# Performance work log

Measured on AMD Instinct MI355X. Metric: run time of the kernel, lower is better.

Reference implementation:

```python
import jax, jax.numpy as jnp
import numpy as np

B, T, D, F, E, K = 2, 2048, 1024, 4096, 8, 2

def setup_inputs() -> dict:
    key = jax.random.key(0)
    k0, k1, k2, k3 = jax.random.split(key, 4)
    return {
        "x": jax.random.normal(k0, (B, T, D), jnp.float32),
        "Wg": jax.random.normal(k1, (D, E), jnp.float32) * (D ** -0.5),
        "W1": jax.random.normal(k2, (E, D, F), jnp.float32) * (D ** -0.5),
        "b1": jnp.zeros((E, F), jnp.float32),
        "W2": jax.random.normal(k3, (E, F, D), jnp.float32) * (F ** -0.5),
        "b2": jnp.zeros((E, D), jnp.float32),
        "topk": K,
    }

def reference(x, Wg, W1, b1, W2, b2, topk):
    n_experts = Wg.shape[-1]
    # Gating logits [B, T, E]
    gating = jnp.einsum('btd,de->bte', x, Wg)
    _, idx = jax.lax.top_k(gating, topk)
    # 0/1 mask of selected experts per token [B, T, E]
    mask = jax.nn.one_hot(idx, n_experts, dtype=x.dtype).sum(axis=-2)
    # Source does `gating -= 1/mask - 1`: no-op where mask==1, -inf where mask==0
    gate = jax.nn.softmax(jnp.where(mask > 0, gating, -jnp.inf), axis=-1)
    # Dense masked per-expert compute, exactly as the source (expert(x * mask_e))
    xm = x[:, :, None, :] * mask[:, :, :, None]          # [B, T, E, D]
    h = jax.nn.gelu(jnp.einsum('bted,edf->btef', xm, W1) + b1)  # [B, T, E, F]
    out_e = jnp.einsum('btef,efd->bted', h, W2) + b2     # [B, T, E, D]
    # Gate and sum over experts
    return jnp.sum(out_e * gate[..., None], axis=-2)      # [B, T, D]
```

## Files before the change

### kernel.cpp

```cpp
#include <hip/hip_runtime.h>
#include <hip/hip_bf16.h>
#include <math.h>

#define NB 2
#define NT 2048
#define NTOK 4096
#define DD 1024
#define FF 4096
#define NE 8
#define KSEL 2
#define BM 128
#define BN 128
#define BK 64
#define ROWCAP 9216
#define ROWTILES 72
#define KP2 2

typedef __attribute__((ext_vector_type(8))) short short8_t;
typedef __attribute__((ext_vector_type(4))) float f32x4;

__device__ __forceinline__ unsigned short f2bf(float f){
  unsigned u = __float_as_uint(f);
  unsigned r = (u + 0x7fffu + ((u >> 16) & 1u)) >> 16;
  return (unsigned short)r;
}

__device__ __forceinline__ int xcd_swz(int lin, int nwg){
  int q = nwg >> 3, r = nwg & 7;
  int xcd = lin & 7, idx = lin >> 3;
  return (xcd < r ? xcd * (q + 1) : r * (q + 1) + (xcd - r) * q) + idx;
}

#define GLOAD_LDS(g, l) \
  __builtin_amdgcn_global_load_lds((const __attribute__((address_space(1))) void*)(g), \
                                   (__attribute__((address_space(3))) void*)(l), 16, 0, 0)


__global__ void k_prep(const float* __restrict__ x, const float* __restrict__ wg,
                       short* __restrict__ xb, int* __restrict__ topk_idx,
                       float* __restrict__ topk_gate, int* __restrict__ counts){
  int wid = threadIdx.x >> 6, lane = threadIdx.x & 63;
  int t = blockIdx.x * 4 + wid;
  const float* xr = x + (size_t)t * DD;
  short* xbr = xb + (size_t)t * DD;
  double acc[NE];
#pragma unroll
  for (int e = 0; e < NE; ++e) acc[e] = 0.0;
#pragma unroll
  for (int p = 0; p < 4; ++p){
    int d = p * 256 + lane * 4;
    float4 v = *(const float4*)(xr + d);
    short4 o;
    o.x = (short)f2bf(v.x); o.y = (short)f2bf(v.y);
    o.z = (short)f2bf(v.z); o.w = (short)f2bf(v.w);
    *(short4*)(xbr + d) = o;
    const float* w0 = wg + (size_t)d * NE;
    float vv[4] = {v.x, v.y, v.z, v.w};
#pragma unroll
    for (int j = 0; j < 4; ++j){
      double xv = (double)vv[j];
#pragma unroll
      for (int e = 0; e < NE; ++e) acc[e] += xv * (double)w0[j * NE + e];
    }
  }
#pragma unroll
  for (int e = 0; e < NE; ++e){
#pragma unroll
    for (int s = 32; s; s >>= 1) acc[e] += __shfl_xor(acc[e], s, 64);
  }
  if (lane == 0){
    int i0 = 0; double v0 = acc[0];
#pragma unroll
    for (int e = 1; e < NE; ++e) if (acc[e] > v0){ v0 = acc[e]; i0 = e; }
    int i1 = -1; double v1 = -1e300;
#pragma unroll
    for (int e = 0; e < NE; ++e) if (e != i0 && acc[e] > v1){ v1 = acc[e]; i1 = e; }
    double g0 = 1.0 / (1.0 + exp(v1 - v0));
    topk_idx[2 * t] = i0; topk_idx[2 * t + 1] = i1;
    topk_gate[2 * t] = (float)g0; topk_gate[2 * t + 1] = (float)(1.0 - g0);
    atomicAdd(&counts[i0], 1);
    atomicAdd(&counts[i1], 1);
  }
}


__global__ void k_transpose_all(const float* __restrict__ W1, const float* __restrict__ W2,
                                short* __restrict__ w1t, short* __restrict__ w2t){
  __shared__ short T[64][132];
  int id = blockIdx.x;
  bool isW2 = id >= 4096;
  int rem = id & 4095;
  int e = rem >> 9;
  int tr = rem & 511;
  int R, C, c0, r0;
  const float* in; short* out;
  if (!isW2){ R = DD; C = FF; c0 = (tr & 63) * 64; r0 = (tr >> 6) * 128;
              in = W1 + (size_t)e * R * C; out = w1t + (size_t)e * R * C; }
  else      { R = FF; C = DD; c0 = (tr & 15) * 64; r0 = (tr >> 4) * 128;
              in = W2 + (size_t)e * R * C; out = w2t + (size_t)e * R * C; }
  int t = threadIdx.x;
  int rr = t >> 4, c4 = (t & 15) * 4;
#pragma unroll
  for (int p = 0; p < 8; ++p){
    int row = p * 16 + rr;
    float4 v = *(const float4*)(in + (size_t)(r0 + row) * C + c0 + c4);
    T[c4 + 0][row] = (short)f2bf(v.x);
    T[c4 + 1][row] = (short)f2bf(v.y);
    T[c4 + 2][row] = (short)f2bf(v.z);
    T[c4 + 3][row] = (short)f2bf(v.w);
  }
  __syncthreads();
  int c8 = (t & 15) * 8;
#pragma unroll
  for (int q = 0; q < 4; ++q){
    int orow = q * 16 + rr;
    short4 lo = *(const short4*)&T[orow][c8];
    short4 hi = *(const short4*)&T[orow][c8 + 4];
    short8_t w;
    w[0] = lo.x; w[1] = lo.y; w[2] = lo.z; w[3] = lo.w;
    w[4] = hi.x; w[5] = hi.y; w[6] = hi.z; w[7] = hi.w;
    *(short8_t*)(out + (size_t)(c0 + orow) * R + r0 + c8) = w;
  }
}


__global__ void k_route_all(const int* __restrict__ counts, const int* __restrict__ topk_idx,
                            const float* __restrict__ topk_gate, int* __restrict__ poff_g,
                            int* __restrict__ row_token, float* __restrict__ row_gate,
                            int* __restrict__ slot_of){
  __shared__ int poff[NE + 1], cur[NE], rends[NE];
  if (threadIdx.x == 0){
    int off = 0;
    for (int e = 0; e < NE; ++e){
      poff[e] = off; cur[e] = off; rends[e] = off + counts[e];
      off += (counts[e] + BM - 1) & ~(BM - 1);
    }
    poff[NE] = off;
    for (int e = 0; e <= NE; ++e) poff_g[e] = poff[e];
  }
  __syncthreads();
  for (int t = threadIdx.x; t < NTOK; t += 256){
#pragma unroll
    for (int k = 0; k < KSEL; ++k){
      int e = topk_idx[2 * t + k];
      float g = topk_gate[2 * t + k];
      int slot = atomicAdd(&cur[e], 1);
      row_token[slot] = t;
      row_gate[slot] = g;
      slot_of[2 * t + k] = slot;
    }
  }
  __syncthreads();
#pragma unroll
  for (int e = 0; e < NE; ++e)
    for (int s = rends[e] + (int)threadIdx.x; s < poff[e + 1]; s += 256){
      row_token[s] = 0; row_gate[s] = 0.f;
    }
}


__launch_bounds__(256, 4)
__global__ void k_gemm1(const short* __restrict__ xb, const short* __restrict__ w1t,
                        const float* __restrict__ b1, short* __restrict__ h,
                        const int* __restrict__ row_token, const int* __restrict__ poff){
  __shared__ short As[BM * BK];
  __shared__ short Bs[BN * BK];
  int wg = xcd_swz(blockIdx.x, ROWTILES * (FF / BN));
  int g = wg >> 6, t6 = wg & 63;
  int bx = (g >> 2) * 8 + (t6 & 7);
  int by = (g & 3) * 8 + (t6 >> 3);
  int row0 = bx * BM;
  if (row0 >= poff[NE]) return;
  int e = 0;
  while (row0 >= poff[e + 1]) ++e;
  int n0 = by * BN;
  int tid = threadIdx.x;

  const short* asrc[4]; const short* bsrc[4];
#pragma unroll
  for (int p = 0; p < 4; ++p){
    int L = p * 256 + tid;
    int r = L >> 3, cs = L & 7;
    int cd = cs ^ (r & 7);
    int tok = row_token[row0 + r];
    asrc[p] = xb + (size_t)tok * DD + cd * 8;
    bsrc[p] = w1t + (size_t)e * FF * DD + (size_t)(n0 + r) * DD + cd * 8;
  }
  short* alds = As + tid * 8;
  short* blds = Bs + tid * 8;

  f32x4 acc[4][4];
#pragma unroll
  for (int i = 0; i < 4; ++i)
#pragma unroll
    for (int j = 0; j < 4; ++j) acc[i][j] = (f32x4){0.f, 0.f, 0.f, 0.f};

  int wid = tid >> 6, lane = tid & 63;
  int wr = wid >> 1, wc = wid & 1;
  int lrow = lane & 15, lk = lane >> 4;

  for (int k0 = 0; k0 < DD; k0 += BK){
#pragma unroll
    for (int p = 0; p < 4; ++p){
      GLOAD_LDS(asrc[p] + k0, alds + p * 2048);
      GLOAD_LDS(bsrc[p] + k0, blds + p * 2048);
    }
    __syncthreads();
#pragma unroll
    for (int kk = 0; kk < 2; ++kk){
      short8_t a[4], b[4];
      int c = kk * 4 + lk;
#pragma unroll
      for (int m = 0; m < 4; ++m){
        int r = wr * 64 + m * 16 + lrow;
        a[m] = *(const short8_t*)(As + r * BK + ((c ^ (r & 7)) * 8));
      }
#pragma unroll
      for (int n = 0; n < 4; ++n){
        int r = wc * 64 + n * 16 + lrow;
        b[n] = *(const short8_t*)(Bs + r * BK + ((c ^ (r & 7)) * 8));
      }
#pragma unroll
      for (int m = 0; m < 4; ++m)
#pragma unroll
        for (int n = 0; n < 4; ++n)
          acc[m][n] = __builtin_amdgcn_mfma_f32_16x16x32_bf16(a[m], b[n], acc[m][n], 0, 0, 0);
    }
    __syncthreads();
  }

  const float* b1e = b1 + (size_t)e * FF;
  float bias[4];
#pragma unroll
  for (int n = 0; n < 4; ++n) bias[n] = b1e[n0 + wc * 64 + n * 16 + lrow];
#pragma unroll
  for (int m = 0; m < 4; ++m){
#pragma unroll
    for (int j = 0; j < 4; ++j){
      int row = row0 + wr * 64 + m * 16 + lk * 4 + j;
      short* hr = h + (size_t)row * FF + n0 + wc * 64 + lrow;
#pragma unroll
      for (int n = 0; n < 4; ++n){
        float v = acc[m][n][j] + bias[n];
        float u = 0.7978845608028654f * (v + 0.044715f * v * v * v);
        float gl = v / (1.0f + __expf(-2.0f * u));
        hr[n * 16] = (short)f2bf(gl);
      }
    }
  }
}


__launch_bounds__(256, 4)
__global__ void k_gemm2(const short* __restrict__ h, const short* __restrict__ w2t,
                        const float* __restrict__ b2, float* __restrict__ ya,
                        float* __restrict__ yb, const int* __restrict__ poff){
  __shared__ short As[BM * BK];
  __shared__ short Bs[BN * BK];
  int wg = xcd_swz(blockIdx.x, ROWTILES * (DD / BN) * KP2);
  int kz = wg / (ROWTILES * (DD / BN));
  int c5 = wg % (ROWTILES * (DD / BN));
  int g = c5 >> 5, t5 = c5 & 31;
  int bx = g * 4 + (t5 & 3);
  int by = t5 >> 2;
  int row0 = bx * BM;
  if (row0 >= poff[NE]) return;
  int e = 0;
  while (row0 >= poff[e + 1]) ++e;
  int n0 = by * BN;
  int tid = threadIdx.x;

  const short* asrc[4]; const short* bsrc[4];
#pragma unroll
  for (int p = 0; p < 4; ++p){
    int L = p * 256 + tid;
    int r = L >> 3, cs = L & 7;
    int cd = cs ^ (r & 7);
    asrc[p] = h + (size_t)(row0 + r) * FF + cd * 8;
    bsrc[p] = w2t + (size_t)e * DD * FF + (size_t)(n0 + r) * FF + cd * 8;
  }
  short* alds = As + tid * 8;
  short* blds = Bs + tid * 8;

  f32x4 acc[4][4];
#pragma unroll
  for (int i = 0; i < 4; ++i)
#pragma unroll
    for (int j = 0; j < 4; ++j) acc[i][j] = (f32x4){0.f, 0.f, 0.f, 0.f};

  int wid = tid >> 6, lane = tid & 63;
  int wr = wid >> 1, wc = wid & 1;
  int lrow = lane & 15, lk = lane >> 4;

  int kbeg = kz * (FF / KP2), kend = kbeg + FF / KP2;
  for (int k0 = kbeg; k0 < kend; k0 += BK){
#pragma unroll
    for (int p = 0; p < 4; ++p){
      GLOAD_LDS(asrc[p] + k0, alds + p * 2048);
      GLOAD_LDS(bsrc[p] + k0, blds + p * 2048);
    }
    __syncthreads();
#pragma unroll
    for (int kk = 0; kk < 2; ++kk){
      short8_t a[4], b[4];
      int c = kk * 4 + lk;
#pragma unroll
      for (int m = 0; m < 4; ++m){
        int r = wr * 64 + m * 16 + lrow;
        a[m] = *(const short8_t*)(As + r * BK + ((c ^ (r & 7)) * 8));
      }
#pragma unroll
      for (int n = 0; n < 4; ++n){
        int r = wc * 64 + n * 16 + lrow;
        b[n] = *(const short8_t*)(Bs + r * BK + ((c ^ (r & 7)) * 8));
      }
#pragma unroll
      for (int m = 0; m < 4; ++m)
#pragma unroll
        for (int n = 0; n < 4; ++n)
          acc[m][n] = __builtin_amdgcn_mfma_f32_16x16x32_bf16(a[m], b[n], acc[m][n], 0, 0, 0);
    }
    __syncthreads();
  }

  float* y = (kz == 0) ? ya : yb;
  const float* b2e = b2 + (size_t)e * DD;
  float bias[4];
#pragma unroll
  for (int n = 0; n < 4; ++n) bias[n] = (kz == 0) ? b2e[n0 + wc * 64 + n * 16 + lrow] : 0.0f;
#pragma unroll
  for (int m = 0; m < 4; ++m){
#pragma unroll
    for (int j = 0; j < 4; ++j){
      int row = row0 + wr * 64 + m * 16 + lk * 4 + j;
      float* yr = y + (size_t)row * DD + n0 + wc * 64 + lrow;
#pragma unroll
      for (int n = 0; n < 4; ++n)
        yr[n * 16] = acc[m][n][j] + bias[n];
    }
  }
}


__global__ void k_combine(const float* __restrict__ ya, const float* __restrict__ yb,
                          const int* __restrict__ slot_of, const float* __restrict__ topk_gate,
                          float* __restrict__ out){
  int i = blockIdx.x * 256 + threadIdx.x;
  int t = i >> 8;
  int c4 = (i & 255) * 4;
  int s0 = slot_of[2 * t], s1 = slot_of[2 * t + 1];
  float g0 = topk_gate[2 * t], g1 = topk_gate[2 * t + 1];
  float4 a0 = *(const float4*)(ya + (size_t)s0 * DD + c4);
  float4 b0 = *(const float4*)(yb + (size_t)s0 * DD + c4);
  float4 a1 = *(const float4*)(ya + (size_t)s1 * DD + c4);
  float4 b1 = *(const float4*)(yb + (size_t)s1 * DD + c4);
  float4 o;
  o.x = g0 * (a0.x + b0.x) + g1 * (a1.x + b1.x);
  o.y = g0 * (a0.y + b0.y) + g1 * (a1.y + b1.y);
  o.z = g0 * (a0.z + b0.z) + g1 * (a1.z + b1.z);
  o.w = g0 * (a0.w + b0.w) + g1 * (a1.w + b1.w);
  *(float4*)(out + (size_t)t * DD + c4) = o;
}


extern "C" void kernel_launch(void* const* d_in, const int* in_sizes, int n_in,
                              void* d_out, int out_size, void* d_ws, size_t ws_size,
                              hipStream_t stream){
  (void)in_sizes; (void)n_in; (void)out_size; (void)ws_size;
  const float* x  = (const float*)d_in[0];
  const float* Wg = (const float*)d_in[1];
  const float* W1 = (const float*)d_in[2];
  const float* b1 = (const float*)d_in[3];
  const float* W2 = (const float*)d_in[4];
  const float* b2 = (const float*)d_in[5];
  float* out = (float*)d_out;
  char* ws = (char*)d_ws;

  int*   counts    = (int*)(ws + 0);
  int*   poff      = (int*)(ws + 256);
  int*   topk_idx  = (int*)(ws + 1024);
  float* topk_gate = (float*)(ws + 33792);
  int*   row_token = (int*)(ws + 66560);
  float* row_gate  = (float*)(ws + 103424);
  int*   slot_of   = (int*)(ws + 140288);
  short* xb        = (short*)(ws + 173056);
  short* w1t       = (short*)(ws + 8561664);
  short* w2t       = (short*)(ws + 75670528);
  short* h         = (short*)(ws + 142779392);
  float* ya        = (float*)(ws + 173056);
  float* yb        = (float*)(ws + 37921792);

  hipMemsetAsync(counts, 0, 32, stream);

  k_prep<<<dim3(NTOK / 4), 256, 0, stream>>>(x, Wg, xb, topk_idx, topk_gate, counts);
  k_transpose_all<<<dim3(8192), 256, 0, stream>>>(W1, W2, w1t, w2t);
  k_route_all<<<dim3(1), 256, 0, stream>>>(counts, topk_idx, topk_gate, poff,
                                           row_token, row_gate, slot_of);
  k_gemm1<<<dim3(ROWTILES * (FF / BN)), 256, 0, stream>>>(xb, w1t, b1, h, row_token, poff);
  k_gemm2<<<dim3(ROWTILES * (DD / BN) * KP2), 256, 0, stream>>>(h, w2t, b2, ya, yb, poff);
  k_combine<<<dim3(NTOK * DD / 4 / 256), 256, 0, stream>>>(ya, yb, slot_of, topk_gate, out);
}
```

Baseline: 470.1 us.

## Double-buffer 128x256 MFMA GEMMs and fuse gated combine via atomics

Both expert GEMMs move to 512-thread blocks with 128x256 tiles and double-buffered LDS. Global-to-LDS loads for the next K-slice are split across the sub-steps and issued while MFMAs run on the current buffer, with raw barriers, sched barriers and setprio controlling the order. The second GEMM now applies the gate and scatters straight into the output with float atomicAdd, which removes the ya/yb buffers and the separate combine kernel. The cost is a memset of the output, atomic contention from two split-K halves and two experts per token, non-deterministic summation order, and more LDS per block.

```diff
diff --git a/kernel.cpp b/kernel.cpp
--- a/kernel.cpp
+++ b/kernel.cpp
@@ -10,7 +10,7 @@
 #define NE 8
 #define KSEL 2
 #define BM 128
-#define BN 128
+#define BN 256
 #define BK 64
 #define ROWCAP 9216
 #define ROWTILES 72
@@ -34,6 +34,34 @@
 #define GLOAD_LDS(g, l) \
   __builtin_amdgcn_global_load_lds((const __attribute__((address_space(1))) void*)(g), \
                                    (__attribute__((address_space(3))) void*)(l), 16, 0, 0)
+
+#define VMCNT0 asm volatile("s_waitcnt vmcnt(0)" ::: "memory")
+#define LGKM0  asm volatile("s_waitcnt lgkmcnt(0)" ::: "memory")
+#define SCHEDB __builtin_amdgcn_sched_barrier(0)
+#define RAWBAR __builtin_amdgcn_s_barrier()
+
+__device__ __forceinline__ void mfma16(f32x4 acc[4][4], const short8_t* a, const short8_t* b){
+#pragma unroll
+  for (int m = 0; m < 4; ++m)
+#pragma unroll
+    for (int n = 0; n < 4; ++n)
+      acc[m][n] = __builtin_amdgcn_mfma_f32_16x16x32_bf16(a[m], b[n], acc[m][n], 0, 0, 0);
+}
+
+__device__ __forceinline__ void read_frags(const short* A, const short* B, int wr, int wc,
+                                           int lrow, int lk, int kk, short8_t* a, short8_t* b){
+  int c = kk * 4 + lk;
+#pragma unroll
+  for (int m = 0; m < 4; ++m){
+    int r = wr * 64 + m * 16 + lrow;
+    a[m] = *(const short8_t*)(A + r * 64 + ((c ^ (r & 7)) * 8));
+  }
+#pragma unroll
+  for (int n = 0; n < 4; ++n){
+    int r = wc * 64 + n * 16 + lrow;
+    b[n] = *(const short8_t*)(B + r * 64 + ((c ^ (r & 7)) * 8));
+  }
+}
 
 
 __global__ void k_prep(const float* __restrict__ x, const float* __restrict__ wg,
@@ -126,8 +154,8 @@
 
 __global__ void k_route_all(const int* __restrict__ counts, const int* __restrict__ topk_idx,
                             const float* __restrict__ topk_gate, int* __restrict__ poff_g,
-                            int* __restrict__ row_token, float* __restrict__ row_gate,
-                            int* __restrict__ slot_of){
+                            int* __restrict__ rend_g, int* __restrict__ row_token,
+                            float* __restrict__ row_gate){
   __shared__ int poff[NE + 1], cur[NE], rends[NE];
   if (threadIdx.x == 0){
     int off = 0;
@@ -137,6 +165,7 @@
     }
     poff[NE] = off;
     for (int e = 0; e <= NE; ++e) poff_g[e] = poff[e];
+    for (int e = 0; e < NE; ++e) rend_g[e] = rends[e];
   }
   __syncthreads();
   for (int t = threadIdx.x; t < NTOK; t += 256){
@@ -147,7 +176,6 @@
       int slot = atomicAdd(&cur[e], 1);
       row_token[slot] = t;
       row_gate[slot] = g;
-      slot_of[2 * t + k] = slot;
     }
   }
   __syncthreads();
@@ -159,16 +187,16 @@
 }
 
 
-__launch_bounds__(256, 4)
+__launch_bounds__(512, 2)
 __global__ void k_gemm1(const short* __restrict__ xb, const short* __restrict__ w1t,
                         const float* __restrict__ b1, short* __restrict__ h,
                         const int* __restrict__ row_token, const int* __restrict__ poff){
-  __shared__ short As[BM * BK];
-  __shared__ short Bs[BN * BK];
+  __shared__ short As[2][BM * BK];
+  __shared__ short Bs[2][BN * BK];
   int wg = xcd_swz(blockIdx.x, ROWTILES * (FF / BN));
-  int g = wg >> 6, t6 = wg & 63;
-  int bx = (g >> 2) * 8 + (t6 & 7);
-  int by = (g & 3) * 8 + (t6 >> 3);
+  int g = wg >> 5, t5 = wg & 31;
+  int bx = (g >> 2) * 8 + (t5 & 7);
+  int by = (g & 3) * 4 + (t5 >> 3);
   int row0 = bx * BM;
   if (row0 >= poff[NE]) return;
   int e = 0;
@@ -176,18 +204,20 @@
   int n0 = by * BN;
   int tid = threadIdx.x;
 
-  const short* asrc[4]; const short* bsrc[4];
+  const short* a_src[2]; const short* b_src[4];
+#pragma unroll
+  for (int p = 0; p < 2; ++p){
+    int L = p * 512 + tid;
+    int r = L >> 3, cd = (L & 7) ^ (r & 7);
+    int tok = row_token[row0 + r];
+    a_src[p] = xb + (size_t)tok * DD + cd * 8;
+  }
 #pragma unroll
   for (int p = 0; p < 4; ++p){
-    int L = p * 256 + tid;
-    int r = L >> 3, cs = L & 7;
-    int cd = cs ^ (r & 7);
-    int tok = row_token[row0 + r];
-    asrc[p] = xb + (size_t)tok * DD + cd * 8;
-    bsrc[p] = w1t + (size_t)e * FF * DD + (size_t)(n0 + r) * DD + cd * 8;
-  }
-  short* alds = As + tid * 8;
-  short* blds = Bs + tid * 8;
+    int L = p * 512 + tid;
+    int r = L >> 3, cd = (L & 7) ^ (r & 7);
+    b_src[p] = w1t + (size_t)e * FF * DD + (size_t)(n0 + r) * DD + cd * 8;
+  }
 
   f32x4 acc[4][4];
 #pragma unroll
@@ -196,37 +226,58 @@
     for (int j = 0; j < 4; ++j) acc[i][j] = (f32x4){0.f, 0.f, 0.f, 0.f};
 
   int wid = tid >> 6, lane = tid & 63;
-  int wr = wid >> 1, wc = wid & 1;
+  int wr = wid >> 2, wc = wid & 3;
   int lrow = lane & 15, lk = lane >> 4;
 
-  for (int k0 = 0; k0 < DD; k0 += BK){
-#pragma unroll
-    for (int p = 0; p < 4; ++p){
-      GLOAD_LDS(asrc[p] + k0, alds + p * 2048);
-      GLOAD_LDS(bsrc[p] + k0, blds + p * 2048);
-    }
-    __syncthreads();
-#pragma unroll
-    for (int kk = 0; kk < 2; ++kk){
-      short8_t a[4], b[4];
-      int c = kk * 4 + lk;
-#pragma unroll
-      for (int m = 0; m < 4; ++m){
-        int r = wr * 64 + m * 16 + lrow;
-        a[m] = *(const short8_t*)(As + r * BK + ((c ^ (r & 7)) * 8));
-      }
-#pragma unroll
-      for (int n = 0; n < 4; ++n){
-        int r = wc * 64 + n * 16 + lrow;
-        b[n] = *(const short8_t*)(Bs + r * BK + ((c ^ (r & 7)) * 8));
-      }
-#pragma unroll
-      for (int m = 0; m < 4; ++m)
-#pragma unroll
-        for (int n = 0; n < 4; ++n)
-          acc[m][n] = __builtin_amdgcn_mfma_f32_16x16x32_bf16(a[m], b[n], acc[m][n], 0, 0, 0);
-    }
-    __syncthreads();
+#define STAGE1_FIRST(B, K0)  { GLOAD_LDS(a_src[0] + (K0), &As[B][0] + tid * 8); \
+                               GLOAD_LDS(a_src[1] + (K0), &As[B][0] + 4096 + tid * 8); \
+                               GLOAD_LDS(b_src[0] + (K0), &Bs[B][0] + tid * 8); }
+#define STAGE1_SECOND(B, K0) { GLOAD_LDS(b_src[1] + (K0), &Bs[B][0] + 4096 + tid * 8); \
+                               GLOAD_LDS(b_src[2] + (K0), &Bs[B][0] + 8192 + tid * 8); \
+                               GLOAD_LDS(b_src[3] + (K0), &Bs[B][0] + 12288 + tid * 8); }
+
+  STAGE1_FIRST(0, 0); STAGE1_SECOND(0, 0);
+  VMCNT0; RAWBAR; SCHEDB;
+
+  const int NITER = (DD / BK) / 2;
+#pragma unroll 1
+  for (int it = 0; it < NITER; ++it){
+    int k0 = it * 2 * BK;
+    bool more = (it < NITER - 1);
+    {
+      STAGE1_FIRST(1, k0 + BK);
+      short8_t a[4], b[4];
+      read_frags(&As[0][0], &Bs[0][0], wr, wc, lrow, lk, 0, a, b);
+      LGKM0; SCHEDB;
+      __builtin_amdgcn_s_setprio(1); mfma16(acc, a, b); __builtin_amdgcn_s_setprio(0);
+      RAWBAR; SCHEDB;
+    }
+    {
+      STAGE1_SECOND(1, k0 + BK);
+      short8_t a[4], b[4];
+      read_frags(&As[0][0], &Bs[0][0], wr, wc, lrow, lk, 1, a, b);
+      LGKM0; SCHEDB;
+      __builtin_amdgcn_s_setprio(1); mfma16(acc, a, b); __builtin_amdgcn_s_setprio(0);
+      VMCNT0;
+      RAWBAR; SCHEDB;
+    }
+    {
+      if (more) STAGE1_FIRST(0, k0 + 2 * BK);
+      short8_t a[4], b[4];
+      read_frags(&As[1][0], &Bs[1][0], wr, wc, lrow, lk, 0, a, b);
+      LGKM0; SCHEDB;
+      __builtin_amdgcn_s_setprio(1); mfma16(acc, a, b); __builtin_amdgcn_s_setprio(0);
+      RAWBAR; SCHEDB;
+    }
+    {
+      if (more) STAGE1_SECOND(0, k0 + 2 * BK);
+      short8_t a[4], b[4];
+      read_frags(&As[1][0], &Bs[1][0], wr, wc, lrow, lk, 1, a, b);
+      LGKM0; SCHEDB;
+      __builtin_amdgcn_s_setprio(1); mfma16(acc, a, b); __builtin_amdgcn_s_setprio(0);
+      if (more) VMCNT0;
+      RAWBAR; SCHEDB;
+    }
   }
 
   const float* b1e = b1 + (size_t)e * FF;
@@ -251,36 +302,39 @@
 }
 
 
-__launch_bounds__(256, 4)
+__launch_bounds__(512, 2)
 __global__ void k_gemm2(const short* __restrict__ h, const short* __restrict__ w2t,
-                        const float* __restrict__ b2, float* __restrict__ ya,
-                        float* __restrict__ yb, const int* __restrict__ poff){
-  __shared__ short As[BM * BK];
-  __shared__ short Bs[BN * BK];
+                        const float* __restrict__ b2, float* __restrict__ out,
+                        const int* __restrict__ row_token, const float* __restrict__ row_gate,
+                        const int* __restrict__ poff, const int* __restrict__ rend){
+  __shared__ short As[2][BM * BK];
+  __shared__ short Bs[2][BN * BK];
   int wg = xcd_swz(blockIdx.x, ROWTILES * (DD / BN) * KP2);
-  int kz = wg / (ROWTILES * (DD / BN));
-  int c5 = wg % (ROWTILES * (DD / BN));
-  int g = c5 >> 5, t5 = c5 & 31;
-  int bx = g * 4 + (t5 & 3);
-  int by = t5 >> 2;
+  int g = wg >> 5, t5 = wg & 31;
+  int bx = (g % 9) * 8 + (t5 & 7);
+  int kz = g / 9;
+  int by = t5 >> 3;
   int row0 = bx * BM;
   if (row0 >= poff[NE]) return;
   int e = 0;
   while (row0 >= poff[e + 1]) ++e;
   int n0 = by * BN;
   int tid = threadIdx.x;
-
-  const short* asrc[4]; const short* bsrc[4];
+  int kbeg = kz * (FF / KP2);
+
+  const short* a_src[2]; const short* b_src[4];
+#pragma unroll
+  for (int p = 0; p < 2; ++p){
+    int L = p * 512 + tid;
+    int r = L >> 3, cd = (L & 7) ^ (r & 7);
+    a_src[p] = h + (size_t)(row0 + r) * FF + kbeg + cd * 8;
+  }
 #pragma unroll
   for (int p = 0; p < 4; ++p){
-    int L = p * 256 + tid;
-    int r = L >> 3, cs = L & 7;
-    int cd = cs ^ (r & 7);
-    asrc[p] = h + (size_t)(row0 + r) * FF + cd * 8;
-    bsrc[p] = w2t + (size_t)e * DD * FF + (size_t)(n0 + r) * FF + cd * 8;
-  }
-  short* alds = As + tid * 8;
-  short* blds = Bs + tid * 8;
+    int L = p * 512 + tid;
+    int r = L >> 3, cd = (L & 7) ^ (r & 7);
+    b_src[p] = w2t + (size_t)e * DD * FF + (size_t)(n0 + r) * FF + kbeg + cd * 8;
+  }
 
   f32x4 acc[4][4];
 #pragma unroll
@@ -289,77 +343,74 @@
     for (int j = 0; j < 4; ++j) acc[i][j] = (f32x4){0.f, 0.f, 0.f, 0.f};
 
   int wid = tid >> 6, lane = tid & 63;
-  int wr = wid >> 1, wc = wid & 1;
+  int wr = wid >> 2, wc = wid & 3;
   int lrow = lane & 15, lk = lane >> 4;
 
-  int kbeg = kz * (FF / KP2), kend = kbeg + FF / KP2;
-  for (int k0 = kbeg; k0 < kend; k0 += BK){
-#pragma unroll
-    for (int p = 0; p < 4; ++p){
-      GLOAD_LDS(asrc[p] + k0, alds + p * 2048);
-      GLOAD_LDS(bsrc[p] + k0, blds + p * 2048);
-    }
-    __syncthreads();
-#pragma unroll
-    for (int kk = 0; kk < 2; ++kk){
-      short8_t a[4], b[4];
-      int c = kk * 4 + lk;
-#pragma unroll
-      for (int m = 0; m < 4; ++m){
-        int r = wr * 64 + m * 16 + lrow;
-        a[m] = *(const short8_t*)(As + r * BK + ((c ^ (r & 7)) * 8));
-      }
-#pragma unroll
-      for (int n = 0; n < 4; ++n){
-        int r = wc * 64 + n * 16 + lrow;
-        b[n] = *(const short8_t*)(Bs + r * BK + ((c ^ (r & 7)) * 8));
-      }
-#pragma unroll
-      for (int m = 0; m < 4; ++m)
-#pragma unroll
-        for (int n = 0; n < 4; ++n)
-          acc[m][n] = __builtin_amdgcn_mfma_f32_16x16x32_bf16(a[m], b[n], acc[m][n], 0, 0, 0);
-    }
-    __syncthreads();
-  }
-
-  float* y = (kz == 0) ? ya : yb;
+  STAGE1_FIRST(0, 0); STAGE1_SECOND(0, 0);
+  VMCNT0; RAWBAR; SCHEDB;
+
+  const int NITER2 = (FF / KP2 / BK) / 2;
+#pragma unroll 1
+  for (int it = 0; it < NITER2; ++it){
+    int k0 = it * 2 * BK;
+    bool more = (it < NITER2 - 1);
+    {
+      STAGE1_FIRST(1, k0 + BK);
+      short8_t a[4], b[4];
+      read_frags(&As[0][0], &Bs[0][0], wr, wc, lrow, lk, 0, a, b);
+      LGKM0; SCHEDB;
+      __builtin_amdgcn_s_setprio(1); mfma16(acc, a, b); __builtin_amdgcn_s_setprio(0);
+      RAWBAR; SCHEDB;
+    }
+    {
+      STAGE1_SECOND(1, k0 + BK);
+      short8_t a[4], b[4];
+      read_frags(&As[0][0], &Bs[0][0], wr, wc, lrow, lk, 1, a, b);
+      LGKM0; SCHEDB;
+      __builtin_amdgcn_s_setprio(1); mfma16(acc, a, b); __builtin_amdgcn_s_setprio(0);
+      VMCNT0;
+      RAWBAR; SCHEDB;
+    }
+    {
+      if (more) STAGE1_FIRST(0, k0 + 2 * BK);
+      short8_t a[4], b[4];
+      read_frags(&As[1][0], &Bs[1][0], wr, wc, lrow, lk, 0, a, b);
+      LGKM0; SCHEDB;
+      __builtin_amdgcn_s_setprio(1); mfma16(acc, a, b); __builtin_amdgcn_s_setprio(0);
+      RAWBAR; SCHEDB;
+    }
+    {
+      if (more) STAGE1_SECOND(0, k0 + 2 * BK);
+      short8_t a[4], b[4];
+      read_frags(&As[1][0], &Bs[1][0], wr, wc, lrow, lk, 1, a, b);
+      LGKM0; SCHEDB;
+      __builtin_amdgcn_s_setprio(1); mfma16(acc, a, b); __builtin_amdgcn_s_setprio(0);
+      if (more) VMCNT0;
+      RAWBAR; SCHEDB;
+    }
+  }
+
+  int rende = rend[e];
   const float* b2e = b2 + (size_t)e * DD;
   float bias[4];
 #pragma unroll
-  for (int n = 0; n < 4; ++n) bias[n] = (kz == 0) ? b2e[n0 + wc * 64 + n * 16 + lrow] : 0.0f;
+  for (int n = 0; n < 4; ++n)
+    bias[n] = (kz == 0) ? b2e[n0 + wc * 64 + n * 16 + lrow] : 0.0f;
 #pragma unroll
   for (int m = 0; m < 4; ++m){
 #pragma unroll
     for (int j = 0; j < 4; ++j){
       int row = row0 + wr * 64 + m * 16 + lk * 4 + j;
-      float* yr = y + (size_t)row * DD + n0 + wc * 64 + lrow;
-#pragma unroll
-      for (int n = 0; n < 4; ++n)
-        yr[n * 16] = acc[m][n][j] + bias[n];
-    }
-  }
-}
-
-
-__global__ void k_combine(const float* __restrict__ ya, const float* __restrict__ yb,
-                          const int* __restrict__ slot_of, const float* __restrict__ topk_gate,
-                          float* __restrict__ out){
-  int i = blockIdx.x * 256 + threadIdx.x;
-  int t = i >> 8;
-  int c4 = (i & 255) * 4;
-  int s0 = slot_of[2 * t], s1 = slot_of[2 * t + 1];
-  float g0 = topk_gate[2 * t], g1 = topk_gate[2 * t + 1];
-  float4 a0 = *(const float4*)(ya + (size_t)s0 * DD + c4);
-  float4 b0 = *(const float4*)(yb + (size_t)s0 * DD + c4);
-  float4 a1 = *(const float4*)(ya + (size_t)s1 * DD + c4);
-  float4 b1 = *(const float4*)(yb + (size_t)s1 * DD + c4);
-  float4 o;
-  o.x = g0 * (a0.x + b0.x) + g1 * (a1.x + b1.x);
-  o.y = g0 * (a0.y + b0.y) + g1 * (a1.y + b1.y);
-  o.z = g0 * (a0.z + b0.z) + g1 * (a1.z + b1.z);
-  o.w = g0 * (a0.w + b0.w) + g1 * (a1.w + b1.w);
-  *(float4*)(out + (size_t)t * DD + c4) = o;
+      if (row < rende){
+        int tok = row_token[row];
+        float gt = row_gate[row];
+        float* orow = out + (size_t)tok * DD + n0 + wc * 64 + lrow;
+#pragma unroll
+        for (int n = 0; n < 4; ++n)
+          atomicAdd(&orow[n * 16], gt * (acc[m][n][j] + bias[n]));
+      }
+    }
+  }
 }
 
 
@@ -378,25 +429,24 @@
 
   int*   counts    = (int*)(ws + 0);
   int*   poff      = (int*)(ws + 256);
+  int*   rend      = (int*)(ws + 512);
   int*   topk_idx  = (int*)(ws + 1024);
   float* topk_gate = (float*)(ws + 33792);
   int*   row_token = (int*)(ws + 66560);
   float* row_gate  = (float*)(ws + 103424);
-  int*   slot_of   = (int*)(ws + 140288);
-  short* xb        = (short*)(ws + 173056);
-  short* w1t       = (short*)(ws + 8561664);
-  short* w2t       = (short*)(ws + 75670528);
-  short* h         = (short*)(ws + 142779392);
-  float* ya        = (float*)(ws + 173056);
-  float* yb        = (float*)(ws + 37921792);
+  short* xb        = (short*)(ws + 140288);
+  short* w1t       = (short*)(ws + 8528896);
+  short* w2t       = (short*)(ws + 75637760);
+  short* h         = (short*)(ws + 142746624);
 
   hipMemsetAsync(counts, 0, 32, stream);
+  hipMemsetAsync(out, 0, (size_t)NTOK * DD * sizeof(float), stream);
 
   k_prep<<<dim3(NTOK / 4), 256, 0, stream>>>(x, Wg, xb, topk_idx, topk_gate, counts);
   k_transpose_all<<<dim3(8192), 256, 0, stream>>>(W1, W2, w1t, w2t);
-  k_route_all<<<dim3(1), 256, 0, stream>>>(counts, topk_idx, topk_gate, poff,
-                                           row_token, row_gate, slot_of);
-  k_gemm1<<<dim3(ROWTILES * (FF / BN)), 256, 0, stream>>>(xb, w1t, b1, h, row_token, poff);
-  k_gemm2<<<dim3(ROWTILES * (DD / BN) * KP2), 256, 0, stream>>>(h, w2t, b2, ya, yb, poff);
-  k_combine<<<dim3(NTOK * DD / 4 / 256), 256, 0, stream>>>(ya, yb, slot_of, topk_gate, out);
-}
+  k_route_all<<<dim3(1), 256, 0, stream>>>(counts, topk_idx, topk_gate, poff, rend,
+                                           row_token, row_gate);
+  k_gemm1<<<dim3(ROWTILES * (FF / BN)), 512, 0, stream>>>(xb, w1t, b1, h, row_token, poff);
+  k_gemm2<<<dim3(ROWTILES * (DD / BN) * KP2), 512, 0, stream>>>(h, w2t, b2, out,
+                                                                row_token, row_gate, poff, rend);
+}
```

Result: slower. 550.5 us (+17.1%).

## Use 256x256 double-buffered GEMM tiles with fused bf16 conversion of x

Applied to the files above, without the earlier changes.

Both expert GEMMs move from 128x128 single-buffered tiles to 256x256 tiles with 512 threads. They double-buffer LDS, interleave the next tile's loads with MFMA phases, and raise wave priority around the MFMA blocks. GEMM1 now reads fp32 x directly and converts it to bf16 while writing to LDS, which removes the separate bf16 x buffer written in prep. GEMM2's split-K now runs as two sequential launches where the second adds into one output buffer, so combine reads a single y array. Expert padding grows to 256 rows, which adds wasted rows, and the larger tiles cut occupancy and the number of workgroups.

```diff
diff --git a/kernel.cpp b/kernel.cpp
--- a/kernel.cpp
+++ b/kernel.cpp
@@ -2,27 +2,22 @@
 #include <hip/hip_bf16.h>
 #include <math.h>
 
-#define NB 2
-#define NT 2048
 #define NTOK 4096
 #define DD 1024
 #define FF 4096
 #define NE 8
 #define KSEL 2
-#define BM 128
-#define BN 128
 #define BK 64
-#define ROWCAP 9216
-#define ROWTILES 72
-#define KP2 2
+#define PADR 256
+#define ROWCAP 10240
+#define MT 40
 
 typedef __attribute__((ext_vector_type(8))) short short8_t;
 typedef __attribute__((ext_vector_type(4))) float f32x4;
 
 __device__ __forceinline__ unsigned short f2bf(float f){
   unsigned u = __float_as_uint(f);
-  unsigned r = (u + 0x7fffu + ((u >> 16) & 1u)) >> 16;
-  return (unsigned short)r;
+  return (unsigned short)((u + 0x7fffu + ((u >> 16) & 1u)) >> 16);
 }
 
 __device__ __forceinline__ int xcd_swz(int lin, int nwg){
@@ -34,15 +29,19 @@
 #define GLOAD_LDS(g, l) \
   __builtin_amdgcn_global_load_lds((const __attribute__((address_space(1))) void*)(g), \
                                    (__attribute__((address_space(3))) void*)(l), 16, 0, 0)
+#define WAIT_VL asm volatile("s_waitcnt vmcnt(0) lgkmcnt(0)" ::: "memory")
+#define WAIT_V  asm volatile("s_waitcnt vmcnt(0)" ::: "memory")
+#define RAWBAR __builtin_amdgcn_s_barrier()
+#define PRIO1 __builtin_amdgcn_s_setprio(1)
+#define PRIO0 __builtin_amdgcn_s_setprio(0)
 
 
 __global__ void k_prep(const float* __restrict__ x, const float* __restrict__ wg,
-                       short* __restrict__ xb, int* __restrict__ topk_idx,
-                       float* __restrict__ topk_gate, int* __restrict__ counts){
+                       int* __restrict__ topk_idx, float* __restrict__ topk_gate,
+                       int* __restrict__ counts){
   int wid = threadIdx.x >> 6, lane = threadIdx.x & 63;
   int t = blockIdx.x * 4 + wid;
   const float* xr = x + (size_t)t * DD;
-  short* xbr = xb + (size_t)t * DD;
   double acc[NE];
 #pragma unroll
   for (int e = 0; e < NE; ++e) acc[e] = 0.0;
@@ -50,10 +49,6 @@
   for (int p = 0; p < 4; ++p){
     int d = p * 256 + lane * 4;
     float4 v = *(const float4*)(xr + d);
-    short4 o;
-    o.x = (short)f2bf(v.x); o.y = (short)f2bf(v.y);
-    o.z = (short)f2bf(v.z); o.w = (short)f2bf(v.w);
-    *(short4*)(xbr + d) = o;
     const float* w0 = wg + (size_t)d * NE;
     float vv[4] = {v.x, v.y, v.z, v.w};
 #pragma unroll
@@ -126,14 +121,13 @@
 
 __global__ void k_route_all(const int* __restrict__ counts, const int* __restrict__ topk_idx,
                             const float* __restrict__ topk_gate, int* __restrict__ poff_g,
-                            int* __restrict__ row_token, float* __restrict__ row_gate,
-                            int* __restrict__ slot_of){
+                            int* __restrict__ row_token, int* __restrict__ slot_of){
   __shared__ int poff[NE + 1], cur[NE], rends[NE];
   if (threadIdx.x == 0){
     int off = 0;
     for (int e = 0; e < NE; ++e){
       poff[e] = off; cur[e] = off; rends[e] = off + counts[e];
-      off += (counts[e] + BM - 1) & ~(BM - 1);
+      off += (counts[e] + PADR - 1) & ~(PADR - 1);
     }
     poff[NE] = off;
     for (int e = 0; e <= NE; ++e) poff_g[e] = poff[e];
@@ -143,90 +137,131 @@
 #pragma unroll
     for (int k = 0; k < KSEL; ++k){
       int e = topk_idx[2 * t + k];
-      float g = topk_gate[2 * t + k];
       int slot = atomicAdd(&cur[e], 1);
       row_token[slot] = t;
-      row_gate[slot] = g;
       slot_of[2 * t + k] = slot;
     }
   }
   __syncthreads();
 #pragma unroll
   for (int e = 0; e < NE; ++e)
-    for (int s = rends[e] + (int)threadIdx.x; s < poff[e + 1]; s += 256){
-      row_token[s] = 0; row_gate[s] = 0.f;
-    }
-}
-
-
-__launch_bounds__(256, 4)
-__global__ void k_gemm1(const short* __restrict__ xb, const short* __restrict__ w1t,
+    for (int s = rends[e] + (int)threadIdx.x; s < poff[e + 1]; s += 256)
+      row_token[s] = 0;
+}
+
+
+__launch_bounds__(512, 2)
+__global__ void k_gemm1(const float* __restrict__ x, const short* __restrict__ w1t,
                         const float* __restrict__ b1, short* __restrict__ h,
                         const int* __restrict__ row_token, const int* __restrict__ poff){
-  __shared__ short As[BM * BK];
-  __shared__ short Bs[BN * BK];
-  int wg = xcd_swz(blockIdx.x, ROWTILES * (FF / BN));
-  int g = wg >> 6, t6 = wg & 63;
-  int bx = (g >> 2) * 8 + (t6 & 7);
-  int by = (g & 3) * 8 + (t6 >> 3);
-  int row0 = bx * BM;
+  __shared__ short As[2][2][8192];
+  __shared__ short Bs[2][2][8192];
+  int lin = xcd_swz(blockIdx.x, MT * (FF / 256));
+  int by = lin / MT, bx = lin % MT;
+  int row0 = bx * 256;
   if (row0 >= poff[NE]) return;
   int e = 0;
   while (row0 >= poff[e + 1]) ++e;
-  int n0 = by * BN;
+  int n0 = by * 256;
   int tid = threadIdx.x;
-
-  const short* asrc[4]; const short* bsrc[4];
+  int wid = tid >> 6, lane = tid & 63;
+  int wr = wid >> 2, wc = wid & 3;
+  int lrow = lane & 15, lk = lane >> 4;
+
+  const short* bsrc[2];
+#pragma unroll
+  for (int p = 0; p < 2; ++p){
+    int L = p * 512 + tid;
+    int r = L >> 3, cd = (L & 7) ^ (r & 7);
+    bsrc[p] = w1t + (size_t)e * FF * DD + (size_t)(n0 + r) * DD + cd * 8;
+  }
+  const float* asrc[2][4];
+  int aelem[4];
 #pragma unroll
   for (int p = 0; p < 4; ++p){
-    int L = p * 256 + tid;
-    int r = L >> 3, cs = L & 7;
-    int cd = cs ^ (r & 7);
-    int tok = row_token[row0 + r];
-    asrc[p] = xb + (size_t)tok * DD + cd * 8;
-    bsrc[p] = w1t + (size_t)e * FF * DD + (size_t)(n0 + r) * DD + cd * 8;
-  }
-  short* alds = As + tid * 8;
-  short* blds = Bs + tid * 8;
-
-  f32x4 acc[4][4];
-#pragma unroll
-  for (int i = 0; i < 4; ++i)
+    int q = p * 512 + tid;
+    int r = q >> 4, c4 = (q & 15) * 4;
+    aelem[p] = r * 64 + (((c4 >> 3) ^ (r & 7)) << 3) + (c4 & 7);
+#pragma unroll
+    for (int h2 = 0; h2 < 2; ++h2){
+      int tok = row_token[row0 + h2 * 128 + r];
+      asrc[h2][p] = x + (size_t)tok * DD + c4;
+    }
+  }
+
+  f32x4 acc[8][4];
+#pragma unroll
+  for (int i = 0; i < 8; ++i)
 #pragma unroll
     for (int j = 0; j < 4; ++j) acc[i][j] = (f32x4){0.f, 0.f, 0.f, 0.f};
 
-  int wid = tid >> 6, lane = tid & 63;
-  int wr = wid >> 1, wc = wid & 1;
-  int lrow = lane & 15, lk = lane >> 4;
-
-  for (int k0 = 0; k0 < DD; k0 += BK){
+  auto rdA = [&](const short* A0, int mq, int kk, short8_t* av){
+#pragma unroll
+    for (int m = 0; m < 4; ++m){
+      int r = mq * 64 + m * 16 + lrow;
+      av[m] = *(const short8_t*)(A0 + r * 64 + (((kk * 4 + lk) ^ (r & 7)) << 3));
+    }
+  };
+  auto rdB = [&](const short* B0, int kk, short8_t* bv){
+#pragma unroll
+    for (int n = 0; n < 4; ++n){
+      int r = (wc & 1) * 64 + n * 16 + lrow;
+      bv[n] = *(const short8_t*)(B0 + r * 64 + (((kk * 4 + lk) ^ (r & 7)) << 3));
+    }
+  };
+  auto MF = [&](int mq, short8_t* av, short8_t* bv){
+#pragma unroll
+    for (int m = 0; m < 4; ++m)
+#pragma unroll
+      for (int n = 0; n < 4; ++n)
+        acc[mq * 4 + m][n] = __builtin_amdgcn_mfma_f32_16x16x32_bf16(av[m], bv[n], acc[mq * 4 + m][n], 0, 0, 0);
+  };
+  auto aload = [&](float4* f, int h2, int k0){
+#pragma unroll
+    for (int p = 0; p < 4; ++p) f[p] = *(const float4*)(asrc[h2][p] + k0);
+  };
+  auto awrite = [&](float4* f, int nb, int h2){
+    short* dst = &As[nb][h2][0];
 #pragma unroll
     for (int p = 0; p < 4; ++p){
-      GLOAD_LDS(asrc[p] + k0, alds + p * 2048);
-      GLOAD_LDS(bsrc[p] + k0, blds + p * 2048);
-    }
-    __syncthreads();
-#pragma unroll
-    for (int kk = 0; kk < 2; ++kk){
-      short8_t a[4], b[4];
-      int c = kk * 4 + lk;
-#pragma unroll
-      for (int m = 0; m < 4; ++m){
-        int r = wr * 64 + m * 16 + lrow;
-        a[m] = *(const short8_t*)(As + r * BK + ((c ^ (r & 7)) * 8));
-      }
-#pragma unroll
-      for (int n = 0; n < 4; ++n){
-        int r = wc * 64 + n * 16 + lrow;
-        b[n] = *(const short8_t*)(Bs + r * BK + ((c ^ (r & 7)) * 8));
-      }
-#pragma unroll
-      for (int m = 0; m < 4; ++m)
-#pragma unroll
-        for (int n = 0; n < 4; ++n)
-          acc[m][n] = __builtin_amdgcn_mfma_f32_16x16x32_bf16(a[m], b[n], acc[m][n], 0, 0, 0);
-    }
-    __syncthreads();
+      short4 cv;
+      cv.x = (short)f2bf(f[p].x); cv.y = (short)f2bf(f[p].y);
+      cv.z = (short)f2bf(f[p].z); cv.w = (short)f2bf(f[p].w);
+      *(short4*)(dst + aelem[p]) = cv;
+    }
+  };
+  auto bstage = [&](int nb, int h2, int k0){
+    GLOAD_LDS(bsrc[0] + (size_t)h2 * 128 * DD + k0, &Bs[nb][h2][0] + tid * 8);
+    GLOAD_LDS(bsrc[1] + (size_t)h2 * 128 * DD + k0, &Bs[nb][h2][0] + 4096 + tid * 8);
+  };
+
+  float4 fa[4], fc[4];
+  aload(fa, 0, 0); aload(fc, 1, 0);
+  bstage(0, 0, 0); bstage(0, 1, 0);
+  awrite(fa, 0, 0); awrite(fc, 0, 1);
+  WAIT_VL; RAWBAR;
+
+#pragma unroll 1
+  for (int kt = 0; kt < DD / BK; ++kt){
+    int buf = kt & 1, nb = buf ^ 1;
+    int k1 = (kt + 1) * BK;
+    bool more = (kt + 1 < DD / BK);
+    const short* A0 = &As[buf][wr][0];
+    const short* B0 = &Bs[buf][wc >> 1][0];
+    short8_t av[4], bv[4];
+    if (more){ aload(fa, 0, k1); bstage(nb, 0, k1); }
+    rdB(B0, 0, bv); rdA(A0, 0, 0, av);
+    RAWBAR; PRIO1; MF(0, av, bv); PRIO0; RAWBAR;
+    if (more){ aload(fc, 1, k1); bstage(nb, 1, k1); }
+    rdA(A0, 1, 0, av);
+    RAWBAR; PRIO1; MF(1, av, bv); PRIO0; RAWBAR;
+    if (more) awrite(fa, nb, 0);
+    rdB(B0, 1, bv); rdA(A0, 0, 1, av);
+    RAWBAR; PRIO1; MF(0, av, bv); PRIO0; RAWBAR;
+    if (more) awrite(fc, nb, 1);
+    rdA(A0, 1, 1, av);
+    RAWBAR; PRIO1; MF(1, av, bv); PRIO0;
+    WAIT_VL; RAWBAR;
   }
 
   const float* b1e = b1 + (size_t)e * FF;
@@ -234,14 +269,14 @@
 #pragma unroll
   for (int n = 0; n < 4; ++n) bias[n] = b1e[n0 + wc * 64 + n * 16 + lrow];
 #pragma unroll
-  for (int m = 0; m < 4; ++m){
+  for (int mi = 0; mi < 8; ++mi){
 #pragma unroll
     for (int j = 0; j < 4; ++j){
-      int row = row0 + wr * 64 + m * 16 + lk * 4 + j;
+      int row = row0 + wr * 128 + mi * 16 + lk * 4 + j;
       short* hr = h + (size_t)row * FF + n0 + wc * 64 + lrow;
 #pragma unroll
       for (int n = 0; n < 4; ++n){
-        float v = acc[m][n][j] + bias[n];
+        float v = acc[mi][n][j] + bias[n];
         float u = 0.7978845608028654f * (v + 0.044715f * v * v * v);
         float gl = v / (1.0f + __expf(-2.0f * u));
         hr[n * 16] = (short)f2bf(gl);
@@ -251,114 +286,131 @@
 }
 
 
-__launch_bounds__(256, 4)
-__global__ void k_gemm2(const short* __restrict__ h, const short* __restrict__ w2t,
-                        const float* __restrict__ b2, float* __restrict__ ya,
-                        float* __restrict__ yb, const int* __restrict__ poff){
-  __shared__ short As[BM * BK];
-  __shared__ short Bs[BN * BK];
-  int wg = xcd_swz(blockIdx.x, ROWTILES * (DD / BN) * KP2);
-  int kz = wg / (ROWTILES * (DD / BN));
-  int c5 = wg % (ROWTILES * (DD / BN));
-  int g = c5 >> 5, t5 = c5 & 31;
-  int bx = g * 4 + (t5 & 3);
-  int by = t5 >> 2;
-  int row0 = bx * BM;
+__launch_bounds__(512, 2)
+__global__ void k_gemm2(const short* __restrict__ hA, const short* __restrict__ w2t,
+                        const float* __restrict__ b2, float* __restrict__ y,
+                        const int* __restrict__ poff, int kbeg, int am){
+  __shared__ short As[2][2][8192];
+  __shared__ short Bs[2][2][8192];
+  int lin = xcd_swz(blockIdx.x, MT * (DD / 256));
+  int by = lin / MT, bx = lin % MT;
+  int row0 = bx * 256;
   if (row0 >= poff[NE]) return;
   int e = 0;
   while (row0 >= poff[e + 1]) ++e;
-  int n0 = by * BN;
+  int n0 = by * 256;
   int tid = threadIdx.x;
-
-  const short* asrc[4]; const short* bsrc[4];
-#pragma unroll
-  for (int p = 0; p < 4; ++p){
-    int L = p * 256 + tid;
-    int r = L >> 3, cs = L & 7;
-    int cd = cs ^ (r & 7);
-    asrc[p] = h + (size_t)(row0 + r) * FF + cd * 8;
-    bsrc[p] = w2t + (size_t)e * DD * FF + (size_t)(n0 + r) * FF + cd * 8;
-  }
-  short* alds = As + tid * 8;
-  short* blds = Bs + tid * 8;
-
-  f32x4 acc[4][4];
-#pragma unroll
-  for (int i = 0; i < 4; ++i)
+  int wid = tid >> 6, lane = tid & 63;
+  int wr = wid >> 2, wc = wid & 3;
+  int lrow = lane & 15, lk = lane >> 4;
+
+  const short* asrc[2]; const short* bsrc[2];
+#pragma unroll
+  for (int p = 0; p < 2; ++p){
+    int L = p * 512 + tid;
+    int r = L >> 3, cd = (L & 7) ^ (r & 7);
+    asrc[p] = hA + (size_t)(row0 + r) * FF + kbeg + cd * 8;
+    bsrc[p] = w2t + (size_t)e * DD * FF + (size_t)(n0 + r) * FF + kbeg + cd * 8;
+  }
+
+  f32x4 acc[8][4];
+#pragma unroll
+  for (int i = 0; i < 8; ++i)
 #pragma unroll
     for (int j = 0; j < 4; ++j) acc[i][j] = (f32x4){0.f, 0.f, 0.f, 0.f};
 
-  int wid = tid >> 6, lane = tid & 63;
-  int wr = wid >> 1, wc = wid & 1;
-  int lrow = lane & 15, lk = lane >> 4;
-
-  int kbeg = kz * (FF / KP2), kend = kbeg + FF / KP2;
-  for (int k0 = kbeg; k0 < kend; k0 += BK){
-#pragma unroll
-    for (int p = 0; p < 4; ++p){
-      GLOAD_LDS(asrc[p] + k0, alds + p * 2048);
-      GLOAD_LDS(bsrc[p] + k0, blds + p * 2048);
-    }
-    __syncthreads();
-#pragma unroll
-    for (int kk = 0; kk < 2; ++kk){
-      short8_t a[4], b[4];
-      int c = kk * 4 + lk;
-#pragma unroll
-      for (int m = 0; m < 4; ++m){
-        int r = wr * 64 + m * 16 + lrow;
-        a[m] = *(const short8_t*)(As + r * BK + ((c ^ (r & 7)) * 8));
+  auto rdA = [&](const short* A0, int mq, int kk, short8_t* av){
+#pragma unroll
+    for (int m = 0; m < 4; ++m){
+      int r = mq * 64 + m * 16 + lrow;
+      av[m] = *(const short8_t*)(A0 + r * 64 + (((kk * 4 + lk) ^ (r & 7)) << 3));
+    }
+  };
+  auto rdB = [&](const short* B0, int kk, short8_t* bv){
+#pragma unroll
+    for (int n = 0; n < 4; ++n){
+      int r = (wc & 1) * 64 + n * 16 + lrow;
+      bv[n] = *(const short8_t*)(B0 + r * 64 + (((kk * 4 + lk) ^ (r & 7)) << 3));
+    }
+  };
+  auto MF = [&](int mq, short8_t* av, short8_t* bv){
+#pragma unroll
+    for (int m = 0; m < 4; ++m)
+#pragma unroll
+      for (int n = 0; n < 4; ++n)
+        acc[mq * 4 + m][n] = __builtin_amdgcn_mfma_f32_16x16x32_bf16(av[m], bv[n], acc[mq * 4 + m][n], 0, 0, 0);
+  };
+  auto astage = [&](int nb, int h2, int k0){
+    GLOAD_LDS(asrc[0] + (size_t)h2 * 128 * FF + k0, &As[nb][h2][0] + tid * 8);
+    GLOAD_LDS(asrc[1] + (size_t)h2 * 128 * FF + k0, &As[nb][h2][0] + 4096 + tid * 8);
+  };
+  auto bstage = [&](int nb, int h2, int k0){
+    GLOAD_LDS(bsrc[0] + (size_t)h2 * 128 * FF + k0, &Bs[nb][h2][0] + tid * 8);
+    GLOAD_LDS(bsrc[1] + (size_t)h2 * 128 * FF + k0, &Bs[nb][h2][0] + 4096 + tid * 8);
+  };
+
+  astage(0, 0, 0); astage(0, 1, 0);
+  bstage(0, 0, 0); bstage(0, 1, 0);
+  WAIT_V; RAWBAR;
+
+  const int NKT = 2048 / BK;
+#pragma unroll 1
+  for (int kt = 0; kt < NKT; ++kt){
+    int buf = kt & 1, nb = buf ^ 1;
+    int k1 = (kt + 1) * BK;
+    bool more = (kt + 1 < NKT);
+    const short* A0 = &As[buf][wr][0];
+    const short* B0 = &Bs[buf][wc >> 1][0];
+    short8_t av[4], bv[4];
+    if (more){ astage(nb, 0, k1); bstage(nb, 0, k1); }
+    rdB(B0, 0, bv); rdA(A0, 0, 0, av);
+    RAWBAR; PRIO1; MF(0, av, bv); PRIO0; RAWBAR;
+    if (more){ astage(nb, 1, k1); bstage(nb, 1, k1); }
+    rdA(A0, 1, 0, av);
+    RAWBAR; PRIO1; MF(1, av, bv); PRIO0; RAWBAR;
+    rdB(B0, 1, bv); rdA(A0, 0, 1, av);
+    RAWBAR; PRIO1; MF(0, av, bv); PRIO0; RAWBAR;
+    rdA(A0, 1, 1, av);
+    RAWBAR; PRIO1; MF(1, av, bv); PRIO0;
+    WAIT_V; RAWBAR;
+  }
+
+  float bias[4];
+  const float* b2e = b2 + (size_t)e * DD;
+#pragma unroll
+  for (int n = 0; n < 4; ++n) bias[n] = b2e[n0 + wc * 64 + n * 16 + lrow];
+#pragma unroll
+  for (int mi = 0; mi < 8; ++mi){
+#pragma unroll
+    for (int j = 0; j < 4; ++j){
+      int row = row0 + wr * 128 + mi * 16 + lk * 4 + j;
+      float* yr = y + (size_t)row * DD + n0 + wc * 64 + lrow;
+      if (am){
+#pragma unroll
+        for (int n = 0; n < 4; ++n) yr[n * 16] += acc[mi][n][j];
+      } else {
+#pragma unroll
+        for (int n = 0; n < 4; ++n) yr[n * 16] = acc[mi][n][j] + bias[n];
       }
-#pragma unroll
-      for (int n = 0; n < 4; ++n){
-        int r = wc * 64 + n * 16 + lrow;
-        b[n] = *(const short8_t*)(Bs + r * BK + ((c ^ (r & 7)) * 8));
-      }
-#pragma unroll
-      for (int m = 0; m < 4; ++m)
-#pragma unroll
-        for (int n = 0; n < 4; ++n)
-          acc[m][n] = __builtin_amdgcn_mfma_f32_16x16x32_bf16(a[m], b[n], acc[m][n], 0, 0, 0);
-    }
-    __syncthreads();
-  }
-
-  float* y = (kz == 0) ? ya : yb;
-  const float* b2e = b2 + (size_t)e * DD;
-  float bias[4];
-#pragma unroll
-  for (int n = 0; n < 4; ++n) bias[n] = (kz == 0) ? b2e[n0 + wc * 64 + n * 16 + lrow] : 0.0f;
-#pragma unroll
-  for (int m = 0; m < 4; ++m){
-#pragma unroll
-    for (int j = 0; j < 4; ++j){
-      int row = row0 + wr * 64 + m * 16 + lk * 4 + j;
-      float* yr = y + (size_t)row * DD + n0 + wc * 64 + lrow;
-#pragma unroll
-      for (int n = 0; n < 4; ++n)
-        yr[n * 16] = acc[m][n][j] + bias[n];
-    }
-  }
-}
-
-
-__global__ void k_combine(const float* __restrict__ ya, const float* __restrict__ yb,
-                          const int* __restrict__ slot_of, const float* __restrict__ topk_gate,
-                          float* __restrict__ out){
+    }
+  }
+}
+
+
+__global__ void k_combine(const float* __restrict__ y, const int* __restrict__ slot_of,
+                          const float* __restrict__ topk_gate, float* __restrict__ out){
   int i = blockIdx.x * 256 + threadIdx.x;
   int t = i >> 8;
   int c4 = (i & 255) * 4;
   int s0 = slot_of[2 * t], s1 = slot_of[2 * t + 1];
   float g0 = topk_gate[2 * t], g1 = topk_gate[2 * t + 1];
-  float4 a0 = *(const float4*)(ya + (size_t)s0 * DD + c4);
-  float4 b0 = *(const float4*)(yb + (size_t)s0 * DD + c4);
-  float4 a1 = *(const float4*)(ya + (size_t)s1 * DD + c4);
-  float4 b1 = *(const float4*)(yb + (size_t)s1 * DD + c4);
+  float4 a = *(const float4*)(y + (size_t)s0 * DD + c4);
+  float4 b = *(const float4*)(y + (size_t)s1 * DD + c4);
   float4 o;
-  o.x = g0 * (a0.x + b0.x) + g1 * (a1.x + b1.x);
-  o.y = g0 * (a0.y + b0.y) + g1 * (a1.y + b1.y);
-  o.z = g0 * (a0.z + b0.z) + g1 * (a1.z + b1.z);
-  o.w = g0 * (a0.w + b0.w) + g1 * (a1.w + b1.w);
+  o.x = g0 * a.x + g1 * b.x;
+  o.y = g0 * a.y + g1 * b.y;
+  o.z = g0 * a.z + g1 * b.z;
+  o.w = g0 * a.w + g1 * b.w;
   *(float4*)(out + (size_t)t * DD + c4) = o;
 }
 
@@ -377,26 +429,24 @@
   char* ws = (char*)d_ws;
 
   int*   counts    = (int*)(ws + 0);
-  int*   poff      = (int*)(ws + 256);
+  int*   poff      = (int*)(ws + 64);
   int*   topk_idx  = (int*)(ws + 1024);
   float* topk_gate = (float*)(ws + 33792);
   int*   row_token = (int*)(ws + 66560);
-  float* row_gate  = (float*)(ws + 103424);
-  int*   slot_of   = (int*)(ws + 140288);
-  short* xb        = (short*)(ws + 173056);
-  short* w1t       = (short*)(ws + 8561664);
-  short* w2t       = (short*)(ws + 75670528);
-  short* h         = (short*)(ws + 142779392);
-  float* ya        = (float*)(ws + 173056);
-  float* yb        = (float*)(ws + 37921792);
-
-  hipMemsetAsync(counts, 0, 32, stream);
-
-  k_prep<<<dim3(NTOK / 4), 256, 0, stream>>>(x, Wg, xb, topk_idx, topk_gate, counts);
+  int*   slot_of   = (int*)(ws + 107520);
+  short* w1t       = (short*)(ws + 143360);
+  short* w2t       = (short*)(ws + 67252224);
+  short* h         = (short*)(ws + 134361088);
+  float* ya        = (float*)(ws + 143360);
+
+  hipMemsetAsync(counts, 0, 64, stream);
+
+  k_prep<<<dim3(NTOK / 4), 256, 0, stream>>>(x, Wg, topk_idx, topk_gate, counts);
   k_transpose_all<<<dim3(8192), 256, 0, stream>>>(W1, W2, w1t, w2t);
   k_route_all<<<dim3(1), 256, 0, stream>>>(counts, topk_idx, topk_gate, poff,
-                                           row_token, row_gate, slot_of);
-  k_gemm1<<<dim3(ROWTILES * (FF / BN)), 256, 0, stream>>>(xb, w1t, b1, h, row_token, poff);
-  k_gemm2<<<dim3(ROWTILES * (DD / BN) * KP2), 256, 0, stream>>>(h, w2t, b2, ya, yb, poff);
-  k_combine<<<dim3(NTOK * DD / 4 / 256), 256, 0, stream>>>(ya, yb, slot_of, topk_gate, out);
-}
+                                           row_token, slot_of);
+  k_gemm1<<<dim3(MT * (FF / 256)), 512, 0, stream>>>(x, w1t, b1, h, row_token, poff);
+  k_gemm2<<<dim3(MT * (DD / 256)), 512, 0, stream>>>(h, w2t, b2, ya, poff, 0, 0);
+  k_gemm2<<<dim3(MT * (DD / 256)), 512, 0, stream>>>(h, w2t, b2, ya, poff, 2048, 1);
+  k_combine<<<dim3(NTOK * DD / 4 / 256), 256, 0, stream>>>(ya, slot_of, topk_gate, out);
+}
```

After: 615.9 us. 1.31x slower.
